# Performance work log

Hardware: AMD Instinct MI355X
Metric: run time of the kernel (lower is better)

Reference implementation:

```python
import jax, jax.numpy as jnp
import numpy as np

D_MODEL = 1024
NHEAD = 16
DK = D_MODEL // NHEAD
B, LQ, LK = 4, 2048, 2048


def setup_inputs() -> dict:
    key = jax.random.key(0)
    ks = jax.random.split(key, 11)
    s = 1.0 / np.sqrt(D_MODEL)
    inp = {
        "q": jax.random.normal(ks[0], (B, LQ, D_MODEL), jnp.float32),
        "k": jax.random.normal(ks[1], (B, LK, D_MODEL), jnp.float32),
        "v": jax.random.normal(ks[2], (B, LK, D_MODEL), jnp.float32),
        "attn_mask": jnp.triu(jnp.ones((LQ, LK), dtype=bool), k=1),  # True = masked (causal)
        "Wq": jax.random.normal(ks[3], (D_MODEL, D_MODEL), jnp.float32) * s,
        "bq": jnp.zeros((D_MODEL,), jnp.float32),
        "Wk": jax.random.normal(ks[4], (D_MODEL, D_MODEL), jnp.float32) * s,
        "bk": jnp.zeros((D_MODEL,), jnp.float32),
        "Wv": jax.random.normal(ks[5], (D_MODEL, D_MODEL), jnp.float32) * s,
        "bv": jnp.zeros((D_MODEL,), jnp.float32),
        "Wo": jax.random.normal(ks[6], (D_MODEL, D_MODEL), jnp.float32) * s,
        "bo": jnp.zeros((D_MODEL,), jnp.float32),
    }
    return inp


def _split_heads(x, L):
    # (B, L, D) -> (B, H, L, dk)
    return x.reshape(B, L, NHEAD, DK).transpose(0, 2, 1, 3)


def reference(q, k, v, attn_mask, Wq, bq, Wk, bk, Wv, bv, Wo, bo):
    qh = _split_heads(q @ Wq + bq, LQ)
    kh = _split_heads(k @ Wk + bk, LK)
    vh = _split_heads(v @ Wv + bv, LK)
    scale = 1.0 / np.sqrt(DK).astype(np.float32)
    scores = jnp.einsum("bhqd,bhkd->bhqk", qh, kh) * scale
    scores = jnp.where(attn_mask[None, None, :, :], -jnp.inf, scores)
    attn = jax.nn.softmax(scores, axis=-1)
    ctx = jnp.einsum("bhqk,bhkd->bhqd", attn, vh)
    ctx = ctx.transpose(0, 2, 1, 3).reshape(B, LQ, D_MODEL)
    return ctx @ Wo + bo
```

## Files before the change

### kernel.cpp

```cpp
#include <hip/hip_runtime.h>

#define D_MODEL 1024
#define NHEAD 16
#define DKH 64
#define BATCH 4
#define SEQ 2048
#define MROWS (BATCH*SEQ)

typedef unsigned short u16;
typedef __attribute__((ext_vector_type(8))) short bf16x8;
typedef __attribute__((ext_vector_type(4))) float f32x4;

__device__ __forceinline__ u16 f2bf(float f) {
  union { float f; unsigned int u; } x; x.f = f;
  unsigned int r = x.u + 0x7FFFu + ((x.u >> 16) & 1u);
  return (u16)(r >> 16);
}
__device__ __forceinline__ u16 f2bf_fast(float f) {
  union { float f; unsigned int u; } x; x.f = f;
  return (u16)((x.u + 0x7FFFu) >> 16);
}

__device__ __forceinline__ f32x4 mfma16(bf16x8 a, bf16x8 b, f32x4 c) {
  return __builtin_amdgcn_mfma_f32_16x16x32_bf16(a, b, c, 0, 0, 0);
}

__device__ __forceinline__ void gld_lds16(const void* g, void* l) {
  __builtin_amdgcn_global_load_lds((const __attribute__((address_space(1))) unsigned int*)g,
                                   (__attribute__((address_space(3))) unsigned int*)l, 16, 0, 0);
}

__global__ __launch_bounds__(256) void cvt3_kernel(
    const float* __restrict__ q, const float* __restrict__ k, const float* __restrict__ v,
    u16* __restrict__ oq, u16* __restrict__ ok, u16* __restrict__ ov) {
  const int seg = blockIdx.y;
  const float* in = (seg == 0) ? q : (seg == 1) ? k : v;
  u16* out = (seg == 0) ? oq : (seg == 1) ? ok : ov;
  int i = (blockIdx.x * 256 + threadIdx.x) * 4;
  float4 vv = *(const float4*)(in + i);
  ushort4 o;
  o.x = f2bf(vv.x); o.y = f2bf(vv.y); o.z = f2bf(vv.z); o.w = f2bf(vv.w);
  *(ushort4*)(out + i) = o;
}

__global__ __launch_bounds__(256) void transpose_cvt4(
    const float* __restrict__ W0, const float* __restrict__ W1,
    const float* __restrict__ W2, const float* __restrict__ W3,
    u16* __restrict__ T0, u16* __restrict__ T1,
    u16* __restrict__ T2, u16* __restrict__ T3) {
  const int z = blockIdx.z;
  const float* W = (z == 0) ? W0 : (z == 1) ? W1 : (z == 2) ? W2 : W3;
  u16* Wt = (z == 0) ? T0 : (z == 1) ? T1 : (z == 2) ? T2 : T3;
  __shared__ float tile[32][33];
  int bx = blockIdx.x * 32, by = blockIdx.y * 32;
  int tx = threadIdx.x, ty = threadIdx.y;
#pragma unroll
  for (int j = 0; j < 32; j += 8)
    tile[ty + j][tx] = W[(size_t)(by + ty + j) * D_MODEL + bx + tx];
  __syncthreads();
#pragma unroll
  for (int j = 0; j < 32; j += 8)
    Wt[(size_t)(bx + ty + j) * D_MODEL + by + tx] = f2bf(tile[tx][ty + j]);
}

template <typename Epi>
__device__ __forceinline__ void gemm_pipe(const u16* __restrict__ Ap,
                                          const u16* __restrict__ Bp,
                                          int m0, int n0g, Epi epi) {
  __shared__ u16 As[2][128 * 64];
  __shared__ u16 Bs[2][128 * 64];
  const int tid = threadIdx.x;
  const int lane = tid & 63;
  const int w = tid >> 6;
  const int wm = w >> 1, wn = w & 1;
  const int lo = lane & 15, g = lane >> 4;
  const int swz = (lo & 7) << 4;
  const int sg = (tid & 7) ^ ((tid >> 3) & 7);
  const int srow = tid >> 3;

  f32x4 acc[4][4] = {};

  auto STAGE_A = [&](int buf, int tt, int j) {
    int row = j * 32 + srow;
    gld_lds16(Ap + (size_t)(m0 + row) * D_MODEL + tt * 64 + sg * 8,
              &As[buf][j * 2048 + tid * 8]);
  };
  auto STAGE_B = [&](int buf, int tt, int j) {
    int row = j * 32 + srow;
    gld_lds16(Bp + (size_t)(n0g + row) * D_MODEL + tt * 64 + sg * 8,
              &Bs[buf][j * 2048 + tid * 8]);
  };

  STAGE_A(0, 0, 0); STAGE_A(0, 0, 1); STAGE_A(0, 0, 2); STAGE_A(0, 0, 3);
  STAGE_B(0, 0, 0); STAGE_B(0, 0, 1); STAGE_B(0, 0, 2); STAGE_B(0, 0, 3);
  STAGE_B(1, 1, 0); STAGE_B(1, 1, 1); STAGE_B(1, 1, 2); STAGE_B(1, 1, 3);
  asm volatile("s_waitcnt vmcnt(4)" ::: "memory");
  __builtin_amdgcn_s_barrier();

  int cur = 0;
#pragma unroll 1
  for (int t = 0; t < 16; ++t) {
    const int nb = cur ^ 1;
    const char* ab = (const char*)&As[cur][0];
    const char* bb2 = (const char*)&Bs[cur][0];

    bf16x8 bf[4][2], af[2][2];
#pragma unroll
    for (int n = 0; n < 4; ++n) {
      int row = wn * 64 + n * 16 + lo;
      bf[n][0] = *(const bf16x8*)(bb2 + row * 128 + ((g * 16) ^ swz));
      bf[n][1] = *(const bf16x8*)(bb2 + row * 128 + ((64 + g * 16) ^ swz));
    }
#pragma unroll
    for (int m = 0; m < 2; ++m) {
      int row = wm * 64 + m * 16 + lo;
      af[m][0] = *(const bf16x8*)(ab + row * 128 + ((g * 16) ^ swz));
      af[m][1] = *(const bf16x8*)(ab + row * 128 + ((64 + g * 16) ^ swz));
    }
    if (t + 1 < 16) {
      STAGE_A(nb, t + 1, 0); STAGE_A(nb, t + 1, 1);
      STAGE_A(nb, t + 1, 2); STAGE_A(nb, t + 1, 3);
    }
    __builtin_amdgcn_s_barrier();
    __builtin_amdgcn_s_setprio(1);
#pragma unroll
    for (int s2 = 0; s2 < 2; ++s2)
#pragma unroll
      for (int m = 0; m < 2; ++m)
#pragma unroll
        for (int n = 0; n < 4; ++n)
          acc[m][n] = mfma16(af[m][s2], bf[n][s2], acc[m][n]);
    __builtin_amdgcn_s_setprio(0);
    __builtin_amdgcn_s_barrier();

    bf16x8 af2[2][2];
#pragma unroll
    for (int m = 0; m < 2; ++m) {
      int row = wm * 64 + (m + 2) * 16 + lo;
      af2[m][0] = *(const bf16x8*)(ab + row * 128 + ((g * 16) ^ swz));
      af2[m][1] = *(const bf16x8*)(ab + row * 128 + ((64 + g * 16) ^ swz));
    }
    if (t + 2 < 16) {
      STAGE_B(cur, t + 2, 0); STAGE_B(cur, t + 2, 1);
      STAGE_B(cur, t + 2, 2); STAGE_B(cur, t + 2, 3);
    }
    __builtin_amdgcn_s_barrier();
    __builtin_amdgcn_s_setprio(1);
#pragma unroll
    for (int s2 = 0; s2 < 2; ++s2)
#pragma unroll
      for (int m = 0; m < 2; ++m)
#pragma unroll
        for (int n = 0; n < 4; ++n)
          acc[m + 2][n] = mfma16(af2[m][s2], bf[n][s2], acc[m + 2][n]);
    __builtin_amdgcn_s_setprio(0);
    if (t + 2 < 16) asm volatile("s_waitcnt vmcnt(4)" ::: "memory");
    else            asm volatile("s_waitcnt vmcnt(0)" ::: "memory");
    __builtin_amdgcn_s_barrier();
    cur = nb;
  }

  epi(acc, wm, wn, lo, g);
}

__global__ __launch_bounds__(256, 2) void gemm_qkv_kernel(
    const u16* __restrict__ Aq, const u16* __restrict__ Ak, const u16* __restrict__ Av,
    const u16* __restrict__ Wt,
    const float* __restrict__ bq, const float* __restrict__ bk, const float* __restrict__ bv,
    u16* __restrict__ Qhd, u16* __restrict__ Khd, u16* __restrict__ Vhd, float qscale) {
  const int flat = blockIdx.x;
  const int swzb = (flat & 7) * 192 + (flat >> 3);
  const int m0 = (swzb / 24) * 128;
  const int n0g = (swzb % 24) * 128;
  const int chunk = n0g >> 10;
  const u16* Ap = (chunk == 0) ? Aq : (chunk == 1) ? Ak : Av;
  const float* bias = (chunk == 0) ? bq : (chunk == 1) ? bk : bv;
  const float scale = (chunk == 0) ? qscale : 1.0f;

  gemm_pipe(Ap, Wt, m0, n0g,
    [&](f32x4 (&acc)[4][4], int wm, int wn, int lo, int g) {
#pragma unroll
      for (int m = 0; m < 4; ++m)
#pragma unroll
        for (int n = 0; n < 4; ++n) {
          int row0 = m0 + wm * 64 + m * 16 + g * 4;
          int colc = (n0g & 1023) + wn * 64 + n * 16 + lo;
          int hh = colc >> 6, d = colc & 63;
          int bb = row0 >> 11;
          float v0 = (acc[m][n][0] + bias[colc]) * scale;
          float v1 = (acc[m][n][1] + bias[colc]) * scale;
          float v2 = (acc[m][n][2] + bias[colc]) * scale;
          float v3 = (acc[m][n][3] + bias[colc]) * scale;
          if (chunk < 2) {
            u16* out = chunk ? Khd : Qhd;
#pragma unroll
            for (int i = 0; i < 4; ++i) {
              int l = (row0 + i) & 2047;
              float vi = (i == 0) ? v0 : (i == 1) ? v1 : (i == 2) ? v2 : v3;
              out[(((size_t)(bb * NHEAD + hh)) * SEQ + l) * DKH + d] = f2bf(vi);
            }
          } else {
            int l = row0 & 2047;
            int kh = (l >> 2) & 7;
            int pos = (l & ~31) | ((2 * (kh & 3) + (kh >> 2)) << 2);
            ushort4 o;
            o.x = f2bf(v0); o.y = f2bf(v1); o.z = f2bf(v2); o.w = f2bf(v3);
            *(ushort4*)&Vhd[(((size_t)(bb * NHEAD + hh)) * DKH + d) * SEQ + pos] = o;
          }
        }
    });
}

__global__ __launch_bounds__(256, 2) void gemm_o_kernel(
    const u16* __restrict__ A, const u16* __restrict__ Bt,
    const float* __restrict__ bias, float* __restrict__ Cout) {
  const int flat = blockIdx.x;
  const int swzb = (flat & 7) * 64 + (flat >> 3);
  const int m0 = (swzb >> 3) * 128;
  const int n0g = (swzb & 7) * 128;

  gemm_pipe(A, Bt, m0, n0g,
    [&](f32x4 (&acc)[4][4], int wm, int wn, int lo, int g) {
#pragma unroll
      for (int m = 0; m < 4; ++m)
#pragma unroll
        for (int n = 0; n < 4; ++n) {
          int row0 = m0 + wm * 64 + m * 16 + g * 4;
          int col = n0g + wn * 64 + n * 16 + lo;
          float bcol = bias[col];
#pragma unroll
          for (int i = 0; i < 4; ++i)
            Cout[(size_t)(row0 + i) * D_MODEL + col] = acc[m][n][i] + bcol;
        }
    });
}

__global__ __launch_bounds__(256, 3) void attn_kernel(
    const u16* __restrict__ Qh, const u16* __restrict__ Kh,
    const u16* __restrict__ Vt, u16* __restrict__ ctx) {
  const int blk = blockIdx.x;
  const int xcd = blk & 7;
  const int local = blk >> 3;
  const int qb = 15 - (local >> 3);
  const int head = xcd * 8 + (local & 7);
  const int b = head >> 4, h = head & (NHEAD - 1);

  const int tid = threadIdx.x;
  const int lane = tid & 63;
  const int w = tid >> 6;
  const int lo = lane & 15, g = lane >> 4;
  const int swz = (lo & 7) << 4;

  __shared__ u16 Ks[3][64 * 64];
  __shared__ u16 Vs[3][64 * 64];

  const size_t hoff = ((size_t)(b * NHEAD + h)) * SEQ * DKH;
  const u16* Qp = Qh + hoff;
  const u16* Kp = Kh + hoff;
  const u16* Vp = Vt + hoff;

  const int nt = 2 * qb + 2;
  const int qmin = qb * 128 + w * 32;

  bf16x8 aq[2][2];
#pragma unroll
  for (int qs = 0; qs < 2; ++qs)
#pragma unroll
    for (int cc = 0; cc < 2; ++cc)
      aq[qs][cc] = *(const bf16x8*)(Qp + (size_t)(qmin + qs * 16 + lo) * DKH + cc * 32 + g * 8);

  const int r_lo = lane >> 3;
  const int sgr = (lane & 7) ^ r_lo;

  auto STAGE = [&](int buf, int t64) {
#pragma unroll
    for (int j = 0; j < 2; ++j) {
      int row = w * 16 + j * 8 + r_lo;
      gld_lds16(Kp + (size_t)(t64 * 64 + row) * DKH + sgr * 8, &Ks[buf][(w * 2 + j) * 512]);
      gld_lds16(Vp + (size_t)row * SEQ + t64 * 64 + sgr * 8, &Vs[buf][(w * 2 + j) * 512]);
    }
  };

  STAGE(0, 0);
  STAGE(1, 1);
  asm volatile("s_waitcnt vmcnt(0)" ::: "memory");
  __builtin_amdgcn_s_barrier();

  f32x4 c[2][4] = {};
  float m_run[2] = {-1e30f, -1e30f}, l_run[2] = {0.f, 0.f};
  int cur = 0;

  for (int kt = 0; kt < nt; ++kt) {
    int b2 = cur + 2; if (b2 >= 3) b2 -= 3;
    if (kt + 2 < nt) STAGE(b2, kt + 2);

    f32x4 s[2][4] = {};
#pragma unroll
    for (int kn = 0; kn < 4; ++kn) {
      const char* krow = (const char*)&Ks[cur][(kn * 16 + lo) * 64];
#pragma unroll
      for (int cc = 0; cc < 2; ++cc) {
        bf16x8 ak = *(const bf16x8*)(krow + ((cc * 64 + g * 16) ^ swz));
        s[0][kn] = mfma16(ak, aq[0][cc], s[0][kn]);
        s[1][kn] = mfma16(ak, aq[1][cc], s[1][kn]);
      }
    }

    if (kt >= nt - 2) {
#pragma unroll
      for (int qs = 0; qs < 2; ++qs) {
        int q = qmin + qs * 16 + lo;
#pragma unroll
        for (int kn = 0; kn < 4; ++kn)
#pragma unroll
          for (int i = 0; i < 4; ++i) {
            int key = kt * 64 + kn * 16 + g * 4 + i;
            if (key > q) s[qs][kn][i] = -1e30f;
          }
      }
    }

    bf16x8 pb[2][2];
#pragma unroll
    for (int qs = 0; qs < 2; ++qs) {
      float mx = s[qs][0][0];
#pragma unroll
      for (int kn = 0; kn < 4; ++kn)
#pragma unroll
        for (int i = 0; i < 4; ++i) mx = fmaxf(mx, s[qs][kn][i]);
      mx = fmaxf(mx, __shfl_xor(mx, 16));
      mx = fmaxf(mx, __shfl_xor(mx, 32));
      if (!__all(mx - m_run[qs] <= 8.0f)) {
        float mnew = fmaxf(m_run[qs], mx);
        float al = __builtin_amdgcn_exp2f(m_run[qs] - mnew);
        m_run[qs] = mnew;
        l_run[qs] *= al;
#pragma unroll
        for (int dn = 0; dn < 4; ++dn) {
          c[qs][dn][0] *= al; c[qs][dn][1] *= al;
          c[qs][dn][2] *= al; c[qs][dn][3] *= al;
        }
      }
      const float mq = m_run[qs];
      float rs = 0.f;
#pragma unroll
      for (int kn = 0; kn < 4; ++kn)
#pragma unroll
        for (int i = 0; i < 4; ++i) {
          float p = __builtin_amdgcn_exp2f(s[qs][kn][i] - mq);
          s[qs][kn][i] = p;
          rs += p;
        }
      rs += __shfl_xor(rs, 16);
      rs += __shfl_xor(rs, 32);
      l_run[qs] += rs;
#pragma unroll
      for (int kc = 0; kc < 2; ++kc) {
        bf16x8 t;
        t[0] = (short)f2bf_fast(s[qs][2 * kc][0]);
        t[1] = (short)f2bf_fast(s[qs][2 * kc][1]);
        t[2] = (short)f2bf_fast(s[qs][2 * kc][2]);
        t[3] = (short)f2bf_fast(s[qs][2 * kc][3]);
        t[4] = (short)f2bf_fast(s[qs][2 * kc + 1][0]);
        t[5] = (short)f2bf_fast(s[qs][2 * kc + 1][1]);
        t[6] = (short)f2bf_fast(s[qs][2 * kc + 1][2]);
        t[7] = (short)f2bf_fast(s[qs][2 * kc + 1][3]);
        pb[qs][kc] = t;
      }
    }

#pragma unroll
    for (int kc = 0; kc < 2; ++kc)
#pragma unroll
      for (int dn = 0; dn < 4; ++dn) {
        const char* vrow = (const char*)&Vs[cur][(dn * 16 + lo) * 64];
        bf16x8 av = *(const bf16x8*)(vrow + ((kc * 64 + g * 16) ^ swz));
        c[0][dn] = mfma16(av, pb[0][kc], c[0][dn]);
        c[1][dn] = mfma16(av, pb[1][kc], c[1][dn]);
      }

    if (kt + 1 < nt) {
      if (kt + 2 < nt) asm volatile("s_waitcnt vmcnt(4)" ::: "memory");
      else             asm volatile("s_waitcnt vmcnt(0)" ::: "memory");
      __builtin_amdgcn_s_barrier();
    }
    cur = (cur == 2) ? 0 : cur + 1;
  }

#pragma unroll
  for (int qs = 0; qs < 2; ++qs) {
    const float rl = 1.0f / l_run[qs];
    const int q = qmin + qs * 16 + lo;
#pragma unroll
    for (int dn = 0; dn < 4; ++dn) {
      ushort4 o;
      o.x = f2bf(c[qs][dn][0] * rl);
      o.y = f2bf(c[qs][dn][1] * rl);
      o.z = f2bf(c[qs][dn][2] * rl);
      o.w = f2bf(c[qs][dn][3] * rl);
      *(ushort4*)&ctx[((size_t)(b * SEQ + q)) * D_MODEL + h * DKH + dn * 16 + g * 4] = o;
    }
  }
}

extern "C" void kernel_launch(void* const* d_in, const int* in_sizes, int n_in,
                              void* d_out, int out_size, void* d_ws, size_t ws_size,
                              hipStream_t stream) {
  const float* q  = (const float*)d_in[0];
  const float* k  = (const float*)d_in[1];
  const float* v  = (const float*)d_in[2];
  const float* Wq = (const float*)d_in[4];
  const float* bq = (const float*)d_in[5];
  const float* Wk = (const float*)d_in[6];
  const float* bk = (const float*)d_in[7];
  const float* Wv = (const float*)d_in[8];
  const float* bv = (const float*)d_in[9];
  const float* Wo = (const float*)d_in[10];
  const float* bo = (const float*)d_in[11];

  char* ws = (char*)d_ws;
  const size_t MB = 1u << 20;
  u16* qb16 = (u16*)(ws + 0 * MB);
  u16* kb16 = (u16*)(ws + 16 * MB);
  u16* vb16 = (u16*)(ws + 32 * MB);
  u16* Wqkvt = (u16*)(ws + 48 * MB);
  u16* Wot  = (u16*)(ws + 54 * MB);
  u16* Qhd  = (u16*)(ws + 56 * MB);
  u16* Khd  = (u16*)(ws + 72 * MB);
  u16* Vhd  = (u16*)(ws + 88 * MB);
  u16* ctxb = qb16;

  cvt3_kernel<<<dim3(8192, 3), 256, 0, stream>>>(q, k, v, qb16, kb16, vb16);

  u16* Wqt = Wqkvt;
  u16* Wkt = Wqkvt + 1024 * 1024;
  u16* Wvt = Wqkvt + 2 * 1024 * 1024;
  transpose_cvt4<<<dim3(32, 32, 4), dim3(32, 8), 0, stream>>>(
      Wq, Wk, Wv, Wo, Wqt, Wkt, Wvt, Wot);

  const float qscale = 0.125f * 1.4426950408889634f;
  gemm_qkv_kernel<<<1536, 256, 0, stream>>>(qb16, kb16, vb16, Wqkvt,
                                            bq, bk, bv, Qhd, Khd, Vhd, qscale);

  attn_kernel<<<1024, 256, 0, stream>>>(Qhd, Khd, Vhd, ctxb);

  gemm_o_kernel<<<512, 256, 0, stream>>>(ctxb, Wot, bo, (float*)d_out);
}
```

Baseline: 171.6 us.

## Fuse fp32-to-bf16 activation conversion into QKV GEMM A-tile loading

Drops the separate cvt3 kernel that wrote bf16 copies of q, k and v. The QKV GEMM now reads fp32 activations straight into registers, converts them to bf16 and writes them to LDS, while B tiles still use async global-to-LDS loads. This saves one kernel launch and a full read/write pass over the activations. In exchange each GEMM block reads twice the A bytes, and since every A tile is reused across 8 N-tiles the conversion is repeated, which adds VALU work and register pressure to the main loop.

```diff
diff --git a/kernel.cpp b/kernel.cpp
--- a/kernel.cpp
+++ b/kernel.cpp
@@ -28,19 +28,6 @@
 __device__ __forceinline__ void gld_lds16(const void* g, void* l) {
   __builtin_amdgcn_global_load_lds((const __attribute__((address_space(1))) unsigned int*)g,
                                    (__attribute__((address_space(3))) unsigned int*)l, 16, 0, 0);
-}
-
-__global__ __launch_bounds__(256) void cvt3_kernel(
-    const float* __restrict__ q, const float* __restrict__ k, const float* __restrict__ v,
-    u16* __restrict__ oq, u16* __restrict__ ok, u16* __restrict__ ov) {
-  const int seg = blockIdx.y;
-  const float* in = (seg == 0) ? q : (seg == 1) ? k : v;
-  u16* out = (seg == 0) ? oq : (seg == 1) ? ok : ov;
-  int i = (blockIdx.x * 256 + threadIdx.x) * 4;
-  float4 vv = *(const float4*)(in + i);
-  ushort4 o;
-  o.x = f2bf(vv.x); o.y = f2bf(vv.y); o.z = f2bf(vv.z); o.w = f2bf(vv.w);
-  *(ushort4*)(out + i) = o;
 }
 
 __global__ __launch_bounds__(256) void transpose_cvt4(
@@ -61,6 +48,123 @@
 #pragma unroll
   for (int j = 0; j < 32; j += 8)
     Wt[(size_t)(bx + ty + j) * D_MODEL + by + tx] = f2bf(tile[tx][ty + j]);
+}
+
+template <typename Epi>
+__device__ __forceinline__ void gemm_pipe_f32a(const float* __restrict__ Ap32,
+                                               const u16* __restrict__ Bp,
+                                               int m0, int n0g, Epi epi) {
+  __shared__ u16 As[2][128 * 64];
+  __shared__ u16 Bs[2][128 * 64];
+  const int tid = threadIdx.x;
+  const int lane = tid & 63;
+  const int w = tid >> 6;
+  const int wm = w >> 1, wn = w & 1;
+  const int lo = lane & 15, g = lane >> 4;
+  const int swz = (lo & 7) << 4;
+  const int sg = (tid & 7) ^ ((tid >> 3) & 7);
+  const int srow = tid >> 3;
+
+  f32x4 acc[4][4] = {};
+  float4 ar[8];
+
+  auto LOAD_A = [&](int tt) {
+#pragma unroll
+    for (int j = 0; j < 4; ++j) {
+      const float* p = Ap32 + (size_t)(m0 + j * 32 + srow) * D_MODEL + tt * 64 + sg * 8;
+      ar[2 * j] = *(const float4*)p;
+      ar[2 * j + 1] = *(const float4*)(p + 4);
+    }
+  };
+  auto WRITE_A = [&](int buf) {
+#pragma unroll
+    for (int j = 0; j < 4; ++j) {
+      bf16x8 t;
+      t[0] = (short)f2bf(ar[2 * j].x); t[1] = (short)f2bf(ar[2 * j].y);
+      t[2] = (short)f2bf(ar[2 * j].z); t[3] = (short)f2bf(ar[2 * j].w);
+      t[4] = (short)f2bf(ar[2 * j + 1].x); t[5] = (short)f2bf(ar[2 * j + 1].y);
+      t[6] = (short)f2bf(ar[2 * j + 1].z); t[7] = (short)f2bf(ar[2 * j + 1].w);
+      *(bf16x8*)&As[buf][j * 2048 + tid * 8] = t;
+    }
+  };
+  auto STAGE_B = [&](int buf, int tt) {
+#pragma unroll
+    for (int j = 0; j < 4; ++j)
+      gld_lds16(Bp + (size_t)(n0g + j * 32 + srow) * D_MODEL + tt * 64 + sg * 8,
+                &Bs[buf][j * 2048 + tid * 8]);
+  };
+
+  LOAD_A(0);
+  STAGE_B(0, 0);
+  STAGE_B(1, 1);
+  asm volatile("s_waitcnt vmcnt(8)" ::: "memory");
+  WRITE_A(0);
+  asm volatile("s_waitcnt vmcnt(4)" ::: "memory");
+  asm volatile("s_waitcnt lgkmcnt(0)" ::: "memory");
+  __builtin_amdgcn_s_barrier();
+
+  int cur = 0;
+#pragma unroll 1
+  for (int t = 0; t < 16; ++t) {
+    const int nb = cur ^ 1;
+    const char* ab = (const char*)&As[cur][0];
+    const char* bb2 = (const char*)&Bs[cur][0];
+
+    bf16x8 bf[4][2], af[2][2];
+#pragma unroll
+    for (int n = 0; n < 4; ++n) {
+      int row = wn * 64 + n * 16 + lo;
+      bf[n][0] = *(const bf16x8*)(bb2 + row * 128 + ((g * 16) ^ swz));
+      bf[n][1] = *(const bf16x8*)(bb2 + row * 128 + ((64 + g * 16) ^ swz));
+    }
+#pragma unroll
+    for (int m = 0; m < 2; ++m) {
+      int row = wm * 64 + m * 16 + lo;
+      af[m][0] = *(const bf16x8*)(ab + row * 128 + ((g * 16) ^ swz));
+      af[m][1] = *(const bf16x8*)(ab + row * 128 + ((64 + g * 16) ^ swz));
+    }
+    if (t + 1 < 16) LOAD_A(t + 1);
+    __builtin_amdgcn_s_barrier();
+    __builtin_amdgcn_s_setprio(1);
+#pragma unroll
+    for (int s2 = 0; s2 < 2; ++s2)
+#pragma unroll
+      for (int m = 0; m < 2; ++m)
+#pragma unroll
+        for (int n = 0; n < 4; ++n)
+          acc[m][n] = mfma16(af[m][s2], bf[n][s2], acc[m][n]);
+    __builtin_amdgcn_s_setprio(0);
+    __builtin_amdgcn_s_barrier();
+
+    bf16x8 af2[2][2];
+#pragma unroll
+    for (int m = 0; m < 2; ++m) {
+      int row = wm * 64 + (m + 2) * 16 + lo;
+      af2[m][0] = *(const bf16x8*)(ab + row * 128 + ((g * 16) ^ swz));
+      af2[m][1] = *(const bf16x8*)(ab + row * 128 + ((64 + g * 16) ^ swz));
+    }
+    if (t + 2 < 16) STAGE_B(cur, t + 2);
+    __builtin_amdgcn_s_barrier();
+    __builtin_amdgcn_s_setprio(1);
+#pragma unroll
+    for (int s2 = 0; s2 < 2; ++s2)
+#pragma unroll
+      for (int m = 0; m < 2; ++m)
+#pragma unroll
+        for (int n = 0; n < 4; ++n)
+          acc[m + 2][n] = mfma16(af2[m][s2], bf[n][s2], acc[m + 2][n]);
+    __builtin_amdgcn_s_setprio(0);
+    if (t + 1 < 16) {
+      if (t + 2 < 16) asm volatile("s_waitcnt vmcnt(4)" ::: "memory");
+      else            asm volatile("s_waitcnt vmcnt(0)" ::: "memory");
+      WRITE_A(nb);
+      asm volatile("s_waitcnt lgkmcnt(0)" ::: "memory");
+      __builtin_amdgcn_s_barrier();
+    }
+    cur = nb;
+  }
+
+  epi(acc, wm, wn, lo, g);
 }
 
 template <typename Epi>
@@ -164,7 +268,7 @@
 }
 
 __global__ __launch_bounds__(256, 2) void gemm_qkv_kernel(
-    const u16* __restrict__ Aq, const u16* __restrict__ Ak, const u16* __restrict__ Av,
+    const float* __restrict__ Aq, const float* __restrict__ Ak, const float* __restrict__ Av,
     const u16* __restrict__ Wt,
     const float* __restrict__ bq, const float* __restrict__ bk, const float* __restrict__ bv,
     u16* __restrict__ Qhd, u16* __restrict__ Khd, u16* __restrict__ Vhd, float qscale) {
@@ -173,11 +277,11 @@
   const int m0 = (swzb / 24) * 128;
   const int n0g = (swzb % 24) * 128;
   const int chunk = n0g >> 10;
-  const u16* Ap = (chunk == 0) ? Aq : (chunk == 1) ? Ak : Av;
+  const float* Ap = (chunk == 0) ? Aq : (chunk == 1) ? Ak : Av;
   const float* bias = (chunk == 0) ? bq : (chunk == 1) ? bk : bv;
   const float scale = (chunk == 0) ? qscale : 1.0f;
 
-  gemm_pipe(Ap, Wt, m0, n0g,
+  gemm_pipe_f32a(Ap, Wt, m0, n0g,
     [&](f32x4 (&acc)[4][4], int wm, int wn, int lo, int g) {
 #pragma unroll
       for (int m = 0; m < 4; ++m)
@@ -420,17 +524,12 @@
 
   char* ws = (char*)d_ws;
   const size_t MB = 1u << 20;
-  u16* qb16 = (u16*)(ws + 0 * MB);
-  u16* kb16 = (u16*)(ws + 16 * MB);
-  u16* vb16 = (u16*)(ws + 32 * MB);
+  u16* ctxb = (u16*)(ws + 0 * MB);
   u16* Wqkvt = (u16*)(ws + 48 * MB);
   u16* Wot  = (u16*)(ws + 54 * MB);
   u16* Qhd  = (u16*)(ws + 56 * MB);
   u16* Khd  = (u16*)(ws + 72 * MB);
   u16* Vhd  = (u16*)(ws + 88 * MB);
-  u16* ctxb = qb16;
-
-  cvt3_kernel<<<dim3(8192, 3), 256, 0, stream>>>(q, k, v, qb16, kb16, vb16);
 
   u16* Wqt = Wqkvt;
   u16* Wkt = Wqkvt + 1024 * 1024;
@@ -439,7 +538,7 @@
       Wq, Wk, Wv, Wo, Wqt, Wkt, Wvt, Wot);
 
   const float qscale = 0.125f * 1.4426950408889634f;
-  gemm_qkv_kernel<<<1536, 256, 0, stream>>>(qb16, kb16, vb16, Wqkvt,
+  gemm_qkv_kernel<<<1536, 256, 0, stream>>>(q, k, v, Wqkvt,
                                             bq, bk, bv, Qhd, Khd, Vhd, qscale);
 
   attn_kernel<<<1024, 256, 0, stream>>>(Qhd, Khd, Vhd, ctxb);
```

After: 175.5 us. 2.3% more time.
